# Optimization experiments

Measured on AMD Instinct MI355X. Metric: run time of the kernel, lower is better.

The kernel has to match this reference:

```python
import jax, jax.numpy as jnp
import numpy as np

D_MODEL = 1024
NUM_HEADS = 16
HEAD_DIM = D_MODEL // NUM_HEADS


def setup_inputs() -> dict:
    key = jax.random.key(0)
    k_x, k_wqkv, k_bqkv, k_wo, k_bo = jax.random.split(key, 5)
    s = 1.0 / np.sqrt(D_MODEL)
    return {
        "x": jax.random.normal(k_x, (4, 2048, D_MODEL), dtype=jnp.float32),
        "W_qkv": jax.random.uniform(k_wqkv, (D_MODEL, 3 * D_MODEL), jnp.float32, -s, s),
        "b_qkv": jax.random.uniform(k_bqkv, (3 * D_MODEL,), jnp.float32, -s, s),
        "W_out": jax.random.uniform(k_wo, (D_MODEL, D_MODEL), jnp.float32, -s, s),
        "b_out": jax.random.uniform(k_bo, (D_MODEL,), jnp.float32, -s, s),
    }


def reference(x, W_qkv, b_qkv, W_out, b_out):
    B, N, C = x.shape
    # fused QKV projection -> [B, N, 3, H, Dh]
    qkv = (x @ W_qkv + b_qkv).reshape(B, N, 3, NUM_HEADS, HEAD_DIM)
    q = jnp.transpose(qkv[:, :, 0], (0, 2, 1, 3))  # [B, H, N, Dh]
    k = jnp.transpose(qkv[:, :, 1], (0, 2, 1, 3))
    v = jnp.transpose(qkv[:, :, 2], (0, 2, 1, 3))
    scale = 1.0 / jnp.sqrt(jnp.asarray(HEAD_DIM, dtype=x.dtype))
    attn = jnp.einsum('bhqd,bhkd->bhqk', q, k) * scale  # [B, H, N, N]
    attn = jax.nn.softmax(attn, axis=-1)
    # dropout is identity in eval mode
    out = jnp.einsum('bhqk,bhkd->bhqd', attn, v)  # [B, H, N, Dh]
    out = jnp.transpose(out, (0, 2, 1, 3)).reshape(B, N, C)
    return out @ W_out + b_out
```

## Files before the change

kernel.cpp:

```cpp
#include <hip/hip_runtime.h>


typedef __bf16 bf16x8 __attribute__((ext_vector_type(8)));
typedef float f32x4 __attribute__((ext_vector_type(4)));

#define DEV __device__ __forceinline__

DEV unsigned short f2b(float x) {
  unsigned int u = __float_as_uint(x);
  u += 0x7fffu + ((u >> 16) & 1u);
  return (unsigned short)(u >> 16);
}

DEV unsigned int pk_bf16(float a, float b) {
  unsigned int ua = __float_as_uint(a) + 0x8000u;
  unsigned int ub = __float_as_uint(b) + 0x8000u;
  return __builtin_amdgcn_perm(ub, ua, 0x07060302u);
}

#if __has_builtin(__builtin_amdgcn_exp2f)
DEV float exp2_fast(float x) { return __builtin_amdgcn_exp2f(x); }
#else
DEV float exp2_fast(float x) { return exp2f(x); }
#endif

DEV void g2l16(const void* g, void* l) {
  __builtin_amdgcn_global_load_lds(
      (const __attribute__((address_space(1))) unsigned int*)(unsigned long long)g,
      (__attribute__((address_space(3))) unsigned int*)(unsigned int)(unsigned long long)l,
      16, 0, 0);
}

__global__ void cvt_x_kernel(const float* __restrict__ x,
                             unsigned short* __restrict__ xb) {
  int i = blockIdx.x * blockDim.x + threadIdx.x;
  float4 v = ((const float4*)x)[i];
  ushort4 o;
  o.x = f2b(v.x); o.y = f2b(v.y); o.z = f2b(v.z); o.w = f2b(v.w);
  ((ushort4*)xb)[i] = o;
}

__global__ void cvt_wt_kernel(const float* __restrict__ Wq,
                              unsigned short* __restrict__ Wqt,
                              const float* __restrict__ Wo,
                              unsigned short* __restrict__ Wot) {
  __shared__ float tile[32][33];
  int bx = blockIdx.x;
  const float* W;
  unsigned short* Wt;
  int N;
  if (bx < 96) { W = Wq; Wt = Wqt; N = 3072; }
  else         { W = Wo; Wt = Wot; N = 1024; bx -= 96; }
  int n0 = bx * 32, k0 = blockIdx.y * 32;
  int tx = threadIdx.x, ty = threadIdx.y;
#pragma unroll
  for (int i = 0; i < 32; i += 8)
    tile[ty + i][tx] = W[(size_t)(k0 + ty + i) * N + n0 + tx];
  __syncthreads();
#pragma unroll
  for (int i = 0; i < 32; i += 8)
    Wt[(size_t)(n0 + ty + i) * 1024 + k0 + tx] = f2b(tile[tx][ty + i]);
}

#define QSCALE 0.18033688011112042f

template <int MODE>
__global__ __launch_bounds__(256, 2)
void gemm_bt_kernel(const unsigned short* __restrict__ A,
                    const unsigned short* __restrict__ Bt,
                    const float* __restrict__ bias,
                    unsigned short* __restrict__ qout,
                    unsigned short* __restrict__ kfrout,
                    unsigned short* __restrict__ vfrout,
                    float* __restrict__ fout) {
  constexpr int K = 1024;
  __shared__ unsigned short As[128 * 32];
  __shared__ unsigned short Bs[128 * 32];

  const int tid = threadIdx.x;
  const int lane = tid & 63;
  const int w = tid >> 6;
  const int wm = w & 1, wn = w >> 1;
  const int l15 = lane & 15, quad = lane >> 4;
  const int m0 = blockIdx.y * 128;
  const int n0 = blockIdx.x * 128;

  const unsigned short* Ag = A + (size_t)m0 * K;
  const unsigned short* Bg = Bt + (size_t)n0 * K;

  const int c0 = tid, c1 = tid + 256;
  const size_t ga0 = (size_t)(c0 >> 2) * K + (size_t)(c0 & 3) * 8;
  const size_t ga1 = (size_t)(c1 >> 2) * K + (size_t)(c1 & 3) * 8;
  unsigned short* la0 = &As[c0 * 8];
  unsigned short* la1 = &As[c1 * 8];
  unsigned short* lb0 = &Bs[c0 * 8];
  unsigned short* lb1 = &Bs[c1 * 8];

  f32x4 acc[4][4] = {};

  for (int kt = 0; kt < K; kt += 32) {
    g2l16(Ag + ga0 + kt, la0);
    g2l16(Ag + ga1 + kt, la1);
    g2l16(Bg + ga0 + kt, lb0);
    g2l16(Bg + ga1 + kt, lb1);
    __syncthreads();
    bf16x8 af[4], bfr[4];
#pragma unroll
    for (int i = 0; i < 4; ++i) {
      af[i]  = *(const bf16x8*)&As[(wm * 64 + i * 16 + l15) * 32 + quad * 8];
      bfr[i] = *(const bf16x8*)&Bs[(wn * 64 + i * 16 + l15) * 32 + quad * 8];
    }
#pragma unroll
    for (int mi = 0; mi < 4; ++mi)
#pragma unroll
      for (int ni = 0; ni < 4; ++ni)
        acc[mi][ni] = __builtin_amdgcn_mfma_f32_16x16x32_bf16(
            af[mi], bfr[ni], acc[mi][ni], 0, 0, 0);
    __syncthreads();
  }

  float bv[4];
#pragma unroll
  for (int ni = 0; ni < 4; ++ni)
    bv[ni] = bias[n0 + wn * 64 + ni * 16 + l15];

  if (MODE == 0) {
    const int sel = n0 >> 10;
    const int bbat = m0 >> 11;
    const int ktb = ((m0 & 2047) >> 6) + wm;
    if (sel == 0) {
#pragma unroll
      for (int mi = 0; mi < 4; ++mi) {
        int rb = m0 + wm * 64 + mi * 16 + quad * 4;
#pragma unroll
        for (int ni = 0; ni < 4; ++ni) {
          int c = (n0 & 1023) + wn * 64 + ni * 16 + l15;
#pragma unroll
          for (int r = 0; r < 4; ++r)
            qout[(size_t)(rb + r) * 1024 + c] =
                f2b((acc[mi][ni][r] + bv[ni]) * QSCALE);
        }
      }
    } else if (sel == 1) {
#pragma unroll
      for (int ni = 0; ni < 4; ++ni) {
        int c = (n0 & 1023) + wn * 64 + ni * 16 + l15;
        int h = c >> 6, d = c & 63;
        int kc = d >> 5, dq = (d >> 3) & 3, j = d & 7;
        size_t fb = ((((size_t)(bbat * 16 + h) * 32 + ktb) * 8) + kc) * 512 +
                    (size_t)(dq * 16) * 8 + j;
#pragma unroll
        for (int mi = 0; mi < 4; ++mi) {
          size_t fm = fb + (size_t)mi * 1024;
#pragma unroll
          for (int r = 0; r < 4; ++r)
            kfrout[fm + (quad * 4 + r) * 8] = f2b(acc[mi][ni][r] + bv[ni]);
        }
      }
    } else {
      const int fqb = quad >> 1;
      const int jj0 = (quad & 1) * 4;
#pragma unroll
      for (int ni = 0; ni < 4; ++ni) {
        int c = (n0 & 1023) + wn * 64 + ni * 16 + l15;
        int h = c >> 6, d = c & 63;
        int df = d >> 4, fl15 = d & 15;
#pragma unroll
        for (int mi = 0; mi < 4; ++mi) {
          int kc2 = mi >> 1;
          int fquad = (mi & 1) * 2 + fqb;
          size_t fb = ((((size_t)(bbat * 16 + h) * 32 + ktb) * 8) + df * 2 + kc2) * 512 +
                      (size_t)(fquad * 16 + fl15) * 8 + jj0;
          ushort4 pk;
          pk.x = f2b(acc[mi][ni][0] + bv[ni]);
          pk.y = f2b(acc[mi][ni][1] + bv[ni]);
          pk.z = f2b(acc[mi][ni][2] + bv[ni]);
          pk.w = f2b(acc[mi][ni][3] + bv[ni]);
          *(ushort4*)&vfrout[fb] = pk;
        }
      }
    }
  } else {
#pragma unroll
    for (int mi = 0; mi < 4; ++mi) {
      int rb = m0 + wm * 64 + mi * 16 + quad * 4;
#pragma unroll
      for (int ni = 0; ni < 4; ++ni) {
        int c = n0 + wn * 64 + ni * 16 + l15;
#pragma unroll
        for (int r = 0; r < 4; ++r)
          fout[(size_t)(rb + r) * 1024 + c] = acc[mi][ni][r] + bv[ni];
      }
    }
  }
}

__global__ __launch_bounds__(256, 2)
void attn_kernel(const unsigned short* __restrict__ qg,
                 const unsigned short* __restrict__ kfr,
                 const unsigned short* __restrict__ vfr,
                 unsigned short* __restrict__ oat) {
  __shared__ unsigned short pt[256 * 72];

  const int tid = threadIdx.x;
  const int lane = tid & 63;
  const int w = tid >> 6;
  const int l15 = lane & 15, quad = lane >> 4;

  const int head = blockIdx.x * 8 + (blockIdx.y >> 3);
  const int q0 = (blockIdx.y & 7) * 256;
  const int b = head >> 4, h = head & 15;
  const size_t tokbase = (size_t)b * 2048;

  bf16x8 qf[4][2];
#pragma unroll
  for (int ni = 0; ni < 4; ++ni)
#pragma unroll
    for (int kc = 0; kc < 2; ++kc) {
      int q = q0 + w * 64 + ni * 16 + l15;
      qf[ni][kc] = *(const bf16x8*)(qg + (tokbase + q) * 1024 + h * 64 +
                                    kc * 32 + quad * 8);
    }

  f32x4 oacc[4][4] = {};
  float lsum[4] = {0.f, 0.f, 0.f, 0.f};

  const bf16x8* kp = (const bf16x8*)kfr + (size_t)head * 32 * 512;
  const bf16x8* vp = (const bf16x8*)vfr + (size_t)head * 32 * 512;
  const int qrow = w * 64 + l15;

  bf16x8 kfA[8];
#pragma unroll
  for (int f = 0; f < 8; ++f) kfA[f] = kp[f * 64 + lane];

#pragma unroll 2
  for (int kt = 0; kt < 32; ++kt) {
    bf16x8 vfC[8];
    const bf16x8* vc = vp + kt * 512;
#pragma unroll
    for (int f = 0; f < 8; ++f) vfC[f] = vc[f * 64 + lane];

    bf16x8 kfB[8];
    if (kt < 31) {
      const bf16x8* kn = kp + (kt + 1) * 512;
#pragma unroll
      for (int f = 0; f < 8; ++f) kfB[f] = kn[f * 64 + lane];
    }

#pragma unroll
    for (int nh = 0; nh < 2; ++nh) {
      f32x4 st[4][2];
#pragma unroll
      for (int mi = 0; mi < 4; ++mi)
#pragma unroll
        for (int nj = 0; nj < 2; ++nj) {
          f32x4 a = {0.f, 0.f, 0.f, 0.f};
          a = __builtin_amdgcn_mfma_f32_16x16x32_bf16(kfA[mi * 2 + 0], qf[nh * 2 + nj][0], a, 0, 0, 0);
          a = __builtin_amdgcn_mfma_f32_16x16x32_bf16(kfA[mi * 2 + 1], qf[nh * 2 + nj][1], a, 0, 0, 0);
          st[mi][nj] = a;
        }
#pragma unroll
      for (int nj = 0; nj < 2; ++nj) {
        int ni = nh * 2 + nj;
        float rs = 0.f;
#pragma unroll
        for (int mi = 0; mi < 4; ++mi) {
          float p0 = exp2_fast(st[mi][nj][0]);
          float p1 = exp2_fast(st[mi][nj][1]);
          float p2 = exp2_fast(st[mi][nj][2]);
          float p3 = exp2_fast(st[mi][nj][3]);
          rs += (p0 + p1) + (p2 + p3);
          uint2 pw;
          pw.x = pk_bf16(p0, p1);
          pw.y = pk_bf16(p2, p3);
          *(uint2*)&pt[(qrow + ni * 16) * 72 + mi * 16 + quad * 4] = pw;
        }
        lsum[ni] += rs;
      }
    }

    bf16x8 pf[4][2];
#pragma unroll
    for (int ni = 0; ni < 4; ++ni)
#pragma unroll
      for (int kc = 0; kc < 2; ++kc)
        pf[ni][kc] = *(const bf16x8*)&pt[(qrow + ni * 16) * 72 + kc * 32 + quad * 8];
#pragma unroll
    for (int df = 0; df < 4; ++df)
#pragma unroll
      for (int kc = 0; kc < 2; ++kc)
#pragma unroll
        for (int ni = 0; ni < 4; ++ni)
          oacc[df][ni] = __builtin_amdgcn_mfma_f32_16x16x32_bf16(
              vfC[df * 2 + kc], pf[ni][kc], oacc[df][ni], 0, 0, 0);

#pragma unroll
    for (int f = 0; f < 8; ++f) kfA[f] = kfB[f];
  }

#pragma unroll
  for (int ni = 0; ni < 4; ++ni) {
    float s = lsum[ni];
    s += __shfl_xor(s, 16, 64);
    s += __shfl_xor(s, 32, 64);
    float inv = __builtin_amdgcn_rcpf(s);
    int q = q0 + w * 64 + ni * 16 + l15;
#pragma unroll
    for (int df = 0; df < 4; ++df) {
      uint2 pw;
      pw.x = pk_bf16(oacc[df][ni][0] * inv, oacc[df][ni][1] * inv);
      pw.y = pk_bf16(oacc[df][ni][2] * inv, oacc[df][ni][3] * inv);
      *(uint2*)&oat[(tokbase + q) * 1024 + h * 64 + df * 16 + quad * 4] = pw;
    }
  }
}

extern "C" void kernel_launch(void* const* d_in, const int* in_sizes, int n_in,
                              void* d_out, int out_size, void* d_ws, size_t ws_size,
                              hipStream_t stream) {
  const float* x    = (const float*)d_in[0];
  const float* Wqkv = (const float*)d_in[1];
  const float* bqkv = (const float*)d_in[2];
  const float* Wout = (const float*)d_in[3];
  const float* bout = (const float*)d_in[4];
  float* out = (float*)d_out;

  char* ws = (char*)d_ws;
  unsigned short* xb  = (unsigned short*)(ws + (size_t)0);
  unsigned short* wqt = (unsigned short*)(ws + ((size_t)16 << 20));
  unsigned short* wot = (unsigned short*)(ws + ((size_t)22 << 20));
  unsigned short* qbf = (unsigned short*)(ws + ((size_t)24 << 20));
  unsigned short* kfr = (unsigned short*)(ws + ((size_t)40 << 20));
  unsigned short* vfr = (unsigned short*)(ws + ((size_t)56 << 20));
  unsigned short* oat = (unsigned short*)(ws + ((size_t)72 << 20));

  cvt_x_kernel<<<8192, 256, 0, stream>>>(x, xb);
  cvt_wt_kernel<<<dim3(128, 32), dim3(32, 8), 0, stream>>>(Wqkv, wqt, Wout, wot);

  gemm_bt_kernel<0><<<dim3(24, 64), 256, 0, stream>>>(
      xb, wqt, bqkv, qbf, kfr, vfr, nullptr);

  attn_kernel<<<dim3(8, 64), 256, 0, stream>>>(qbf, kfr, vfr, oat);

  gemm_bt_kernel<1><<<dim3(8, 64), 256, 0, stream>>>(
      oat, wot, bout, nullptr, nullptr, nullptr, out);
}
```

Before: 291.3 us.

## Switch attention to 32x32x16 MFMA with smaller query tiles and re-laid-out K/V fragments

The attention kernel now uses 32x32x16 bf16 MFMAs instead of 16x16x32. Each wave handles 32 query rows instead of 64, the block tile shrinks to 128 queries, and the grid doubles. The QKV GEMM epilogue writes K and V fragments in a new layout matching the 32x32 operand format. Occupancy is raised to 4 blocks per CU with half the LDS, and K/V loads are split into half-tile prefetches. The aim is fewer MFMA issues, lower register pressure and better latency hiding, at the cost of loading each K/V tile twice as often across blocks.

```diff
diff --git a/kernel.cpp b/kernel.cpp
--- a/kernel.cpp
+++ b/kernel.cpp
@@ -3,6 +3,7 @@
 
 typedef __bf16 bf16x8 __attribute__((ext_vector_type(8)));
 typedef float f32x4 __attribute__((ext_vector_type(4)));
+typedef float f32x16 __attribute__((ext_vector_type(16)));
 
 #define DEV __device__ __forceinline__
 
@@ -146,37 +147,41 @@
       for (int ni = 0; ni < 4; ++ni) {
         int c = (n0 & 1023) + wn * 64 + ni * 16 + l15;
         int h = c >> 6, d = c & 63;
-        int kc = d >> 5, dq = (d >> 3) & 3, j = d & 7;
-        size_t fb = ((((size_t)(bbat * 16 + h) * 32 + ktb) * 8) + kc) * 512 +
-                    (size_t)(dq * 16) * 8 + j;
+        int fkc = d >> 4;
+        int lhi = (d >> 3) & 1;
+        int j = d & 7;
 #pragma unroll
         for (int mi = 0; mi < 4; ++mi) {
-          size_t fm = fb + (size_t)mi * 1024;
+          int kt32 = mi >> 1;
+          int l31b = (mi & 1) * 16 + quad * 4;
+          size_t base =
+              ((((size_t)(bbat * 16 + h) * 32 + ktb) * 8) + kt32 * 4 + fkc) * 512 +
+              (size_t)(l31b + 32 * lhi) * 8 + j;
 #pragma unroll
           for (int r = 0; r < 4; ++r)
-            kfrout[fm + (quad * 4 + r) * 8] = f2b(acc[mi][ni][r] + bv[ni]);
+            kfrout[base + r * 8] = f2b(acc[mi][ni][r] + bv[ni]);
         }
       }
     } else {
-      const int fqb = quad >> 1;
-      const int jj0 = (quad & 1) * 4;
+      const int lhi = quad >> 1;
+      const int j0 = (quad & 1) * 4;
 #pragma unroll
       for (int ni = 0; ni < 4; ++ni) {
         int c = (n0 & 1023) + wn * 64 + ni * 16 + l15;
         int h = c >> 6, d = c & 63;
-        int df = d >> 4, fl15 = d & 15;
+        int dt = d >> 5;
+        int lp = (d & 31) + 32 * lhi;
 #pragma unroll
         for (int mi = 0; mi < 4; ++mi) {
-          int kc2 = mi >> 1;
-          int fquad = (mi & 1) * 2 + fqb;
-          size_t fb = ((((size_t)(bbat * 16 + h) * 32 + ktb) * 8) + df * 2 + kc2) * 512 +
-                      (size_t)(fquad * 16 + fl15) * 8 + jj0;
+          size_t base =
+              ((((size_t)(bbat * 16 + h) * 32 + ktb) * 8) + dt * 4 + mi) * 512 +
+              (size_t)lp * 8 + j0;
           ushort4 pk;
           pk.x = f2b(acc[mi][ni][0] + bv[ni]);
           pk.y = f2b(acc[mi][ni][1] + bv[ni]);
           pk.z = f2b(acc[mi][ni][2] + bv[ni]);
           pk.w = f2b(acc[mi][ni][3] + bv[ni]);
-          *(ushort4*)&vfrout[fb] = pk;
+          *(ushort4*)&vfrout[base] = pk;
         }
       }
     }
@@ -195,123 +200,126 @@
   }
 }
 
-__global__ __launch_bounds__(256, 2)
+__global__ __launch_bounds__(256, 4)
 void attn_kernel(const unsigned short* __restrict__ qg,
                  const unsigned short* __restrict__ kfr,
                  const unsigned short* __restrict__ vfr,
                  unsigned short* __restrict__ oat) {
-  __shared__ unsigned short pt[256 * 72];
+  __shared__ unsigned short pt[128 * 72];
 
   const int tid = threadIdx.x;
   const int lane = tid & 63;
   const int w = tid >> 6;
-  const int l15 = lane & 15, quad = lane >> 4;
-
-  const int head = blockIdx.x * 8 + (blockIdx.y >> 3);
-  const int q0 = (blockIdx.y & 7) * 256;
+  const int l31 = lane & 31, half = lane >> 5;
+
+  const int head = blockIdx.x * 8 + (blockIdx.y >> 4);
+  const int q0 = (blockIdx.y & 15) * 128;
   const int b = head >> 4, h = head & 15;
   const size_t tokbase = (size_t)b * 2048;
-
-  bf16x8 qf[4][2];
-#pragma unroll
-  for (int ni = 0; ni < 4; ++ni)
-#pragma unroll
-    for (int kc = 0; kc < 2; ++kc) {
-      int q = q0 + w * 64 + ni * 16 + l15;
-      qf[ni][kc] = *(const bf16x8*)(qg + (tokbase + q) * 1024 + h * 64 +
-                                    kc * 32 + quad * 8);
-    }
-
-  f32x4 oacc[4][4] = {};
-  float lsum[4] = {0.f, 0.f, 0.f, 0.f};
+  const int q = q0 + w * 32 + l31;
+
+  bf16x8 qf[4];
+#pragma unroll
+  for (int kc = 0; kc < 4; ++kc)
+    qf[kc] = *(const bf16x8*)(qg + (tokbase + q) * 1024 + h * 64 +
+                              kc * 16 + half * 8);
+
+  f32x16 oacc0 = {};
+  f32x16 oacc1 = {};
+  float lsum = 0.f;
 
   const bf16x8* kp = (const bf16x8*)kfr + (size_t)head * 32 * 512;
   const bf16x8* vp = (const bf16x8*)vfr + (size_t)head * 32 * 512;
-  const int qrow = w * 64 + l15;
-
-  bf16x8 kfA[8];
-#pragma unroll
-  for (int f = 0; f < 8; ++f) kfA[f] = kp[f * 64 + lane];
-
-#pragma unroll 2
+  const int qrow = (w * 32 + l31) * 72;
+
+  bf16x8 kf[4], vf[4];
+#pragma unroll
+  for (int f = 0; f < 4; ++f) {
+    kf[f] = kp[f * 64 + lane];
+    vf[f] = vp[f * 64 + lane];
+  }
+
   for (int kt = 0; kt < 32; ++kt) {
-    bf16x8 vfC[8];
-    const bf16x8* vc = vp + kt * 512;
-#pragma unroll
-    for (int f = 0; f < 8; ++f) vfC[f] = vc[f * 64 + lane];
-
-    bf16x8 kfB[8];
+    const bf16x8* kbase = kp + kt * 512;
+    const bf16x8* vbase = vp + kt * 512;
+
+    f32x16 st = {};
+#pragma unroll
+    for (int kc = 0; kc < 4; ++kc)
+      st = __builtin_amdgcn_mfma_f32_32x32x16_bf16(kf[kc], qf[kc], st, 0, 0, 0);
+
+#pragma unroll
+    for (int f = 0; f < 4; ++f) kf[f] = kbase[(4 + f) * 64 + lane];
+
+#pragma unroll
+    for (int rg = 0; rg < 4; ++rg) {
+      float p0 = exp2_fast(st[rg * 4 + 0]);
+      float p1 = exp2_fast(st[rg * 4 + 1]);
+      float p2 = exp2_fast(st[rg * 4 + 2]);
+      float p3 = exp2_fast(st[rg * 4 + 3]);
+      lsum += (p0 + p1) + (p2 + p3);
+      uint2 pw;
+      pw.x = pk_bf16(p0, p1);
+      pw.y = pk_bf16(p2, p3);
+      *(uint2*)&pt[qrow + 8 * rg + 4 * half] = pw;
+    }
+
+    f32x16 st1 = {};
+#pragma unroll
+    for (int kc = 0; kc < 4; ++kc)
+      st1 = __builtin_amdgcn_mfma_f32_32x32x16_bf16(kf[kc], qf[kc], st1, 0, 0, 0);
+
+#pragma unroll
+    for (int rg = 0; rg < 4; ++rg) {
+      float p0 = exp2_fast(st1[rg * 4 + 0]);
+      float p1 = exp2_fast(st1[rg * 4 + 1]);
+      float p2 = exp2_fast(st1[rg * 4 + 2]);
+      float p3 = exp2_fast(st1[rg * 4 + 3]);
+      lsum += (p0 + p1) + (p2 + p3);
+      uint2 pw;
+      pw.x = pk_bf16(p0, p1);
+      pw.y = pk_bf16(p2, p3);
+      *(uint2*)&pt[qrow + 32 + 8 * rg + 4 * half] = pw;
+    }
+
+    bf16x8 pf[4];
+#pragma unroll
+    for (int kc = 0; kc < 4; ++kc)
+      pf[kc] = *(const bf16x8*)&pt[qrow + kc * 16 + half * 8];
+
+#pragma unroll
+    for (int kc = 0; kc < 4; ++kc)
+      oacc0 = __builtin_amdgcn_mfma_f32_32x32x16_bf16(vf[kc], pf[kc], oacc0, 0, 0, 0);
+
+#pragma unroll
+    for (int f = 0; f < 4; ++f) vf[f] = vbase[(4 + f) * 64 + lane];
+
+#pragma unroll
+    for (int kc = 0; kc < 4; ++kc)
+      oacc1 = __builtin_amdgcn_mfma_f32_32x32x16_bf16(vf[kc], pf[kc], oacc1, 0, 0, 0);
+
     if (kt < 31) {
-      const bf16x8* kn = kp + (kt + 1) * 512;
-#pragma unroll
-      for (int f = 0; f < 8; ++f) kfB[f] = kn[f * 64 + lane];
-    }
-
-#pragma unroll
-    for (int nh = 0; nh < 2; ++nh) {
-      f32x4 st[4][2];
-#pragma unroll
-      for (int mi = 0; mi < 4; ++mi)
-#pragma unroll
-        for (int nj = 0; nj < 2; ++nj) {
-          f32x4 a = {0.f, 0.f, 0.f, 0.f};
-          a = __builtin_amdgcn_mfma_f32_16x16x32_bf16(kfA[mi * 2 + 0], qf[nh * 2 + nj][0], a, 0, 0, 0);
-          a = __builtin_amdgcn_mfma_f32_16x16x32_bf16(kfA[mi * 2 + 1], qf[nh * 2 + nj][1], a, 0, 0, 0);
-          st[mi][nj] = a;
-        }
-#pragma unroll
-      for (int nj = 0; nj < 2; ++nj) {
-        int ni = nh * 2 + nj;
-        float rs = 0.f;
-#pragma unroll
-        for (int mi = 0; mi < 4; ++mi) {
-          float p0 = exp2_fast(st[mi][nj][0]);
-          float p1 = exp2_fast(st[mi][nj][1]);
-          float p2 = exp2_fast(st[mi][nj][2]);
-          float p3 = exp2_fast(st[mi][nj][3]);
-          rs += (p0 + p1) + (p2 + p3);
-          uint2 pw;
-          pw.x = pk_bf16(p0, p1);
-          pw.y = pk_bf16(p2, p3);
-          *(uint2*)&pt[(qrow + ni * 16) * 72 + mi * 16 + quad * 4] = pw;
-        }
-        lsum[ni] += rs;
-      }
-    }
-
-    bf16x8 pf[4][2];
-#pragma unroll
-    for (int ni = 0; ni < 4; ++ni)
-#pragma unroll
-      for (int kc = 0; kc < 2; ++kc)
-        pf[ni][kc] = *(const bf16x8*)&pt[(qrow + ni * 16) * 72 + kc * 32 + quad * 8];
-#pragma unroll
-    for (int df = 0; df < 4; ++df)
-#pragma unroll
-      for (int kc = 0; kc < 2; ++kc)
-#pragma unroll
-        for (int ni = 0; ni < 4; ++ni)
-          oacc[df][ni] = __builtin_amdgcn_mfma_f32_16x16x32_bf16(
-              vfC[df * 2 + kc], pf[ni][kc], oacc[df][ni], 0, 0, 0);
-
-#pragma unroll
-    for (int f = 0; f < 8; ++f) kfA[f] = kfB[f];
-  }
-
-#pragma unroll
-  for (int ni = 0; ni < 4; ++ni) {
-    float s = lsum[ni];
-    s += __shfl_xor(s, 16, 64);
-    s += __shfl_xor(s, 32, 64);
-    float inv = __builtin_amdgcn_rcpf(s);
-    int q = q0 + w * 64 + ni * 16 + l15;
-#pragma unroll
-    for (int df = 0; df < 4; ++df) {
-      uint2 pw;
-      pw.x = pk_bf16(oacc[df][ni][0] * inv, oacc[df][ni][1] * inv);
-      pw.y = pk_bf16(oacc[df][ni][2] * inv, oacc[df][ni][3] * inv);
-      *(uint2*)&oat[(tokbase + q) * 1024 + h * 64 + df * 16 + quad * 4] = pw;
-    }
+#pragma unroll
+      for (int f = 0; f < 4; ++f) {
+        kf[f] = kbase[512 + f * 64 + lane];
+        vf[f] = vbase[512 + f * 64 + lane];
+      }
+    }
+  }
+
+  float s = lsum + __shfl_xor(lsum, 32, 64);
+  float inv = __builtin_amdgcn_rcpf(s);
+  const size_t obase = (tokbase + q) * 1024 + h * 64;
+#pragma unroll
+  for (int rg = 0; rg < 4; ++rg) {
+    int d0 = 8 * rg + 4 * half;
+    uint2 pw;
+    pw.x = pk_bf16(oacc0[rg * 4 + 0] * inv, oacc0[rg * 4 + 1] * inv);
+    pw.y = pk_bf16(oacc0[rg * 4 + 2] * inv, oacc0[rg * 4 + 3] * inv);
+    *(uint2*)&oat[obase + d0] = pw;
+    pw.x = pk_bf16(oacc1[rg * 4 + 0] * inv, oacc1[rg * 4 + 1] * inv);
+    pw.y = pk_bf16(oacc1[rg * 4 + 2] * inv, oacc1[rg * 4 + 3] * inv);
+    *(uint2*)&oat[obase + 32 + d0] = pw;
   }
 }
 
@@ -340,7 +348,7 @@
   gemm_bt_kernel<0><<<dim3(24, 64), 256, 0, stream>>>(
       xb, wqt, bqkv, qbf, kfr, vfr, nullptr);
 
-  attn_kernel<<<dim3(8, 64), 256, 0, stream>>>(qbf, kfr, vfr, oat);
+  attn_kernel<<<dim3(8, 128), 256, 0, stream>>>(qbf, kfr, vfr, oat);
 
   gemm_bt_kernel<1><<<dim3(8, 64), 256, 0, stream>>>(
       oat, wot, bout, nullptr, nullptr, nullptr, out);
```

After: 280.2 us. 3.8% less time.
